# Kernel optimization log

Measured on AMD Instinct MI355X. Metric: run time of the kernel, lower is better.

The kernel has to match this reference:

```python
import jax, jax.numpy as jnp
import numpy as np

MAX_RADIUS = 3.0
NUM_BASIS = 8
NUM_NEIGHBORS = 16.0
N, E, NS, NV, B, D, T, L, HR = 2048, 32768, 32, 16, 8, 32, 32, 2, 64
NW = NS * 2 * NV + NV * 2 * (NS + NV) + NV * 2 * NV  # 3072 per-edge TP weights


def smooth_cutoff(x):
    u = 2.0 * (x - 1.0)
    y = 0.5 * (1.0 - jnp.cos(jnp.pi * u))
    y = jnp.where(u > 0, 0.0, y)
    y = jnp.where(u < -1, 1.0, y)
    return y


def bessel_basis(length):
    # soft_one_hot_linspace(basis='bessel', cutoff=False) * sqrt(NUM_BASIS)
    k = jnp.arange(1, NUM_BASIS + 1, dtype=length.dtype) * jnp.pi
    l = jnp.maximum(length, 1e-9)[..., None]
    return jnp.sqrt(2.0 / MAX_RADIUS) * jnp.sin(k * l / MAX_RADIUS) / l * np.sqrt(NUM_BASIS)


def get_edge_info(x, edge_src, edge_dst):
    n = x.shape[0]
    xr = x.reshape(n, 2, 3)                         # 2 vectors per node
    vec = xr[edge_src] - xr[edge_dst]               # [E,2,3]
    length = jnp.sqrt(jnp.sum(vec * vec, axis=-1) + 1e-12)   # [E,2]
    sh = np.sqrt(3.0) * vec / length[..., None]     # component-normalized l=1 SH
    feat = bessel_basis(length)                     # [E,2,B]
    attr = smooth_cutoff(length / MAX_RADIUS)[..., None] * sh  # [E,2,3]
    return feat.reshape(vec.shape[0], -1), attr


def setup_inputs() -> dict:
    key = jax.random.key(0)
    ks = jax.random.split(key, 20)
    inp = {
        'x': jax.random.normal(ks[0], (N, 6), jnp.float32),
        'batch': jnp.zeros((N,), jnp.int64 if jax.config.jax_enable_x64 else jnp.int32),
        'node_attr': jax.random.randint(ks[1], (N,), 0, T),
        'edge_src': jax.random.randint(ks[2], (E,), 0, N),
        'edge_dst': jax.random.randint(ks[3], (E,), 0, N),
        'emb': jax.random.normal(ks[4], (T, D), jnp.float32),
        'W_uplift': jax.random.normal(ks[5], (NV, 2), jnp.float32),
        'W_sc_s': jax.random.normal(ks[6], (L, NS, D, NS + NV), jnp.float32),
        'W_sc_v': jax.random.normal(ks[7], (L, NV, D, NV), jnp.float32),
        'W_l1_s': jax.random.normal(ks[8], (L, NS, NS), jnp.float32),
        'W_l1_v': jax.random.normal(ks[9], (L, NV, NV), jnp.float32),
        'W_r1': jax.random.normal(ks[10], (L, 2 * B, HR), jnp.float32),
        'W_r2': jax.random.normal(ks[11], (L, HR, NW), jnp.float32),
        'W_l2_s': jax.random.normal(ks[12], (L, NS + NV, NS + NV), jnp.float32),
        'W_l2_v': jax.random.normal(ks[13], (L, NV, NV), jnp.float32),
        'W_si_s': jax.random.normal(ks[14], (L, NS, NS), jnp.float32),
        'W_si_v': jax.random.normal(ks[15], (L, NV, NV), jnp.float32),
        'h': jnp.ones((L,), jnp.float32) * 0.01,
        'mix': jnp.ones((L,), jnp.float32) * 0.5,
    }
    return inp


def reference(x, batch, node_attr, edge_src, edge_dst, emb, W_uplift, W_sc_s, W_sc_v,
              W_l1_s, W_l1_v, W_r1, W_r2, W_l2_s, W_l2_v, W_si_s, W_si_v, h, mix):
    n = x.shape[0]
    a = emb[node_attr]                              # node attr embedding [N,D]
    Q, _ = jnp.linalg.qr(W_uplift)                  # semi-unitary uplift [NV,2]
    y_v = jnp.einsum('ci,nik->nck', Q, x.reshape(n, 2, 3))   # uplift vectors
    y_s = jnp.zeros((n, NS), x.dtype)
    y, y_old = (y_s, y_v), (y_s, y_v)
    n1 = NS * 2 * NV
    n2 = NV * 2 * (NS + NV)
    for i in range(L):
        ef, ea = get_edge_info(x, edge_src, edge_dst)       # [E,2B], [E,2,3]
        ys, yv = y
        # self-connection tensor product (features x node_attr)
        sc_s = jnp.einsum('ni,na,iaj->nj', ys, a, W_sc_s[i]) / np.sqrt(NS * D)
        sc_v = jnp.einsum('nck,na,caj->njk', yv, a, W_sc_v[i]) / np.sqrt(NV * D)
        # lin1
        s1 = ys @ W_l1_s[i] / np.sqrt(NS)
        v1 = jnp.einsum('nck,cj->njk', yv, W_l1_v[i]) / np.sqrt(NV)
        # radial MLP -> per-edge TP weights
        hr = jax.nn.silu(ef @ W_r1[i] / np.sqrt(2 * B))
        w = hr @ W_r2[i] / np.sqrt(HR)                       # [E,NW]
        w_sv = w[:, :n1].reshape(E, NS, 2, NV)
        w_vs = w[:, n1:n1 + n2].reshape(E, NV, 2, NS + NV)
        w_vv = w[:, n1 + n2:].reshape(E, NV, 2, NV)
        s_src, v_src = s1[edge_src], v1[edge_src]
        # edge tensor product: 0e x 1o -> 1o, 1o x 1o -> 0e (dot), 1o x 1o -> 1o (cross)
        e_v = jnp.einsum('esmj,es,emk->ejk', w_sv, s_src, ea) / np.sqrt(NS * 2)
        dots = jnp.einsum('eck,emk->ecm', v_src, ea)
        e_s = jnp.einsum('ecmj,ecm->ej', w_vs, dots) / np.sqrt(NV * 2 * 3)
        crs = jnp.cross(v_src[:, :, None, :], ea[:, None, :, :])  # [E,NV,2,3]
        e_v = e_v + jnp.einsum('ecmj,ecmk->ejk', w_vv, crs) / np.sqrt(NV * 2 * 2)
        # scatter-aggregate over destination nodes
        ns_ = jax.ops.segment_sum(e_s, edge_dst, num_segments=n) / np.sqrt(NUM_NEIGHBORS)
        nv_ = jax.ops.segment_sum(e_v, edge_dst, num_segments=n) / np.sqrt(NUM_NEIGHBORS)
        s2 = ns_ @ W_l2_s[i] / np.sqrt(NS + NV)
        v2 = jnp.einsum('nck,cj->njk', nv_, W_l2_v[i]) / np.sqrt(NV)
        conv_s, conv_v = sc_s + s2, sc_v + v2
        # gate
        g_s = jax.nn.silu(conv_s[:, :NS])
        g_v = jax.nn.sigmoid(conv_s[:, NS:])[:, :, None] * conv_v
        # self-interaction
        si_s = ys @ W_si_s[i] / np.sqrt(NS)
        si_v = jnp.einsum('nck,cj->njk', yv, W_si_v[i]) / np.sqrt(NV)
        # gated leapfrog update
        h2, m = h[i] ** 2, mix[i]
        new_s = 2 * ys - y_old[0] + h2 * (m * g_s + (m - 1) * si_s)
        new_v = 2 * yv - y_old[1] + h2 * (m * g_v + (m - 1) * si_v)
        y_old, y = y, (new_s, new_v)
        x = jnp.einsum('ci,nck->nik', Q, y[1]).reshape(n, 6)  # project back
    return x
```

## Files before the change

kernel.cpp:

```cpp
#include <hip/hip_runtime.h>
#include <hip/hip_bf16.h>
#include <math.h>

#define NN   2048
#define EE   32768
#define NS   32
#define NV   16
#define NB   8
#define DD   32
#define TT   32
#define LL   2
#define HRD  64
#define NWW  3072
#define TPE  128
#define PI_F 3.14159265358979323846f

#define SC_SCS (1.0f/32.0f)
#define SC_SCV 0.04419417382415922f
#define SC_L1S 0.17677669529663687f
#define SC_L1V 0.25f
#define SC_R1  0.25f
#define SC_R2  0.125f
#define SC_ES  0.10206207261596575f
#define SC_EV  0.125f
#define SC_AGG 0.25f
#define SC_L2S 0.14433756729740643f
#define SC_L2V 0.25f
#define SC_SIS 0.17677669529663687f
#define SC_SIV 0.25f

typedef __attribute__((ext_vector_type(8))) short  short8;
typedef __attribute__((ext_vector_type(4))) float  floatx4;

__device__ __forceinline__ floatx4 mfma16(short8 a, short8 b, floatx4 c) {
    return __builtin_amdgcn_mfma_f32_16x16x32_bf16(a, b, c, 0, 0, 0);
}

__device__ __forceinline__ void seg_reduce_store(
        const float (*red)[49], const int* dst_s,
        const int* __restrict__ row_ptr, int ebase,
        int tid, int wave, int lane,
        int* segstart_s, int* wtot_s, int* nseg_s,
        float* __restrict__ outg) {
    int seg_flag = 0, seg_lidx = 0;
    if (tid < TPE) {
        seg_flag = (tid == 0) || (dst_s[tid] != dst_s[tid - 1]);
        unsigned long long m = __ballot(seg_flag != 0);
        if (lane == 0) wtot_s[wave] = (int)__popcll(m);
        seg_lidx = (int)__popcll(m & ((1ull << lane) - 1ull));
    }
    __syncthreads();
    if (seg_flag) segstart_s[seg_lidx + (wave ? wtot_s[0] : 0)] = tid;
    if (tid == 0) {
        int ns = wtot_s[0] + wtot_s[1];
        nseg_s[0] = ns;
        segstart_s[ns] = TPE;
    }
    __syncthreads();
    int nseg = nseg_s[0];
    for (int w = tid; w < nseg * 48; w += 256) {
        int seg = w / 48, c = w - seg * 48;
        int p0 = segstart_s[seg], p1 = segstart_s[seg + 1];
        int d = dst_s[p0];
        float run = 0.f;
        for (int pos = p0; pos < p1; ++pos) run += red[pos][c];
        if (row_ptr[d] >= ebase && row_ptr[d + 1] <= ebase + TPE)
            outg[d * 48 + c] = run;
        else
            atomicAdd(&outg[d * 48 + c], run);
    }
}

__global__ void k_setup(const float* __restrict__ Wup, float* __restrict__ Q,
                        const float* __restrict__ emb,
                        const float* __restrict__ Wscs, const float* __restrict__ Wscv,
                        float* __restrict__ WtS, float* __restrict__ WtV,
                        const float* __restrict__ Wr2, __hip_bfloat16* __restrict__ wr2t,
                        int* __restrict__ deg, int* __restrict__ cursor) {
    int b = blockIdx.x;
    if (b == 0) {
        if (threadIdx.x != 0) return;
        double A[16][2], tau[2];
        for (int i = 0; i < 16; ++i)
            for (int j = 0; j < 2; ++j) A[i][j] = (double)Wup[i*2 + j];
        for (int j = 0; j < 2; ++j) {
            double alpha = A[j][j];
            double xn2 = 0.0;
            for (int i = j + 1; i < 16; ++i) xn2 += A[i][j]*A[i][j];
            if (xn2 == 0.0) {
                tau[j] = 0.0;
            } else {
                double nrm  = sqrt(alpha*alpha + xn2);
                double beta = (alpha >= 0.0) ? -nrm : nrm;
                tau[j] = (beta - alpha) / beta;
                double s = 1.0 / (alpha - beta);
                for (int i = j + 1; i < 16; ++i) A[i][j] *= s;
                A[j][j] = beta;
            }
            for (int k = j + 1; k < 2; ++k) {
                double w = A[j][k];
                for (int i = j + 1; i < 16; ++i) w += A[i][j]*A[i][k];
                w *= tau[j];
                A[j][k] -= w;
                for (int i = j + 1; i < 16; ++i) A[i][k] -= A[i][j]*w;
            }
        }
        double Qm[16][2];
        for (int i = 0; i < 16; ++i)
            for (int j = 0; j < 2; ++j) Qm[i][j] = (i == j) ? 1.0 : 0.0;
        for (int j = 1; j >= 0; --j) {
            for (int k = 0; k < 2; ++k) {
                double w = Qm[j][k];
                for (int i = j + 1; i < 16; ++i) w += A[i][j]*Qm[i][k];
                w *= tau[j];
                Qm[j][k] -= w;
                for (int i = j + 1; i < 16; ++i) Qm[i][k] -= A[i][j]*w;
            }
        }
        for (int i = 0; i < 16; ++i)
            for (int j = 0; j < 2; ++j) Q[i*2 + j] = (float)Qm[i][j];
    } else if (b <= 64) {
        int lt = b - 1;
        int l = lt >> 5, t = lt & 31;
        __shared__ float es[32];
        if (threadIdx.x < 32) es[threadIdx.x] = emb[t*DD + threadIdx.x];
        __syncthreads();
        const float* Ws = Wscs + (size_t)l*NS*DD*48;
        float* oS = WtS + (size_t)(l*TT + t)*NS*48;
        for (int idx = threadIdx.x; idx < NS*48; idx += 256) {
            int i = idx / 48, j = idx % 48;
            float acc = 0.f;
            for (int a = 0; a < 32; ++a) acc += es[a]*Ws[(i*DD + a)*48 + j];
            oS[idx] = acc;
        }
        const float* Wv = Wscv + (size_t)l*NV*DD*NV;
        float* oV = WtV + (size_t)(l*TT + t)*NV*NV;
        for (int idx = threadIdx.x; idx < NV*NV; idx += 256) {
            int c = idx / 16, j = idx % 16;
            float acc = 0.f;
            for (int a = 0; a < 32; ++a) acc += es[a]*Wv[(c*DD + a)*NV + j];
            oV[idx] = acc;
        }
    } else if (b <= 1600) {
        int idx = (b - 65)*256 + threadIdx.x;
        int l = idx / (HRD*NWW);
        int r = idx - l*(HRD*NWW);
        int k = r / NWW;
        int c = r - k*NWW;
        int ch = c >> 6, cc = c & 63, q = cc >> 4, tcc = cc & 15;
        int h = k >> 5, qd = (k >> 3) & 3, j = k & 7;
        size_t dst = (size_t)l*(NWW*HRD)
                   + (size_t)((ch*32 + q*8 + h*4 + qd)*128 + tcc*8 + j);
        wr2t[dst] = __float2bfloat16(Wr2[idx]);
    } else {
        int i = (b - 1601)*256 + threadIdx.x;
        if (i < NN) { deg[i] = 0; cursor[i] = 0; }
    }
}

__global__ void k_hist(const int* __restrict__ edst, int* __restrict__ deg) {
    int e = blockIdx.x*256 + threadIdx.x;
    atomicAdd(&deg[edst[e]], 1);
}

__global__ void k_scan(const int* __restrict__ deg, int* __restrict__ row_ptr) {
    __shared__ int part[256];
    __shared__ int psc[256];
    int t = threadIdx.x;
    int loc[8]; int s = 0;
    for (int k = 0; k < 8; ++k) { loc[k] = deg[t*8 + k]; s += loc[k]; }
    part[t] = s;
    __syncthreads();
    if (t == 0) { int run = 0; for (int i = 0; i < 256; ++i) { psc[i] = run; run += part[i]; } }
    __syncthreads();
    int off = psc[t];
    for (int k = 0; k < 8; ++k) { row_ptr[t*8 + k] = off; off += loc[k]; }
    if (t == 255) row_ptr[2048] = off;
}

__global__ void k_fill(const int* __restrict__ esrc, const int* __restrict__ edst,
                       const int* __restrict__ row_ptr, int* __restrict__ cursor,
                       int* __restrict__ invperm, int* __restrict__ srcs, int* __restrict__ dsts,
                       const float* __restrict__ xin, const float* __restrict__ Q,
                       float* __restrict__ ys0, float* __restrict__ yv0,
                       float* __restrict__ ys1, float* __restrict__ yv1,
                       float* __restrict__ xcur) {
    if (blockIdx.x < 128) {
        int e = blockIdx.x*256 + threadIdx.x;
        int d = edst[e];
        int pos = atomicAdd(&cursor[d], 1);
        int p = row_ptr[d] + pos;
        invperm[e] = p;
        srcs[p] = esrc[e];
        dsts[p] = d;
    } else {
        int n = (blockIdx.x - 128)*256 + threadIdx.x;
        float xl[6];
        for (int i = 0; i < 6; ++i) { xl[i] = xin[n*6 + i]; xcur[n*6 + i] = xl[i]; }
        for (int j = 0; j < 32; ++j) { ys0[n*32 + j] = 0.f; ys1[n*32 + j] = 0.f; }
        for (int c = 0; c < 16; ++c)
            for (int k = 0; k < 3; ++k) {
                float v = Q[c*2 + 0]*xl[k] + Q[c*2 + 1]*xl[3 + k];
                yv0[n*48 + c*3 + k] = v;
                yv1[n*48 + c*3 + k] = v;
            }
    }
}

__global__ void __launch_bounds__(256) k_pre(
        const float* __restrict__ xcur,
        const int* __restrict__ esrc, const int* __restrict__ edst,
        const int* __restrict__ invperm,
        const float* __restrict__ Wr1l,
        __hip_bfloat16* __restrict__ hrg, float* __restrict__ eag,
        const float* __restrict__ ys, const float* __restrict__ yv,
        const float* __restrict__ Wl1s, const float* __restrict__ Wl1v,
        float* __restrict__ s1, float* __restrict__ v1,
        float* __restrict__ nsb, float* __restrict__ nsb2,
        float* __restrict__ nvba, float* __restrict__ nvbb) {
    if (blockIdx.x < 128) {
        __shared__ float Wr1[16*64];
        for (int i = threadIdx.x; i < 16*64; i += 256) Wr1[i] = Wr1l[i];
        __syncthreads();
        int e = blockIdx.x*256 + threadIdx.x;
        int s = esrc[e], d = edst[e];
        int p = invperm[e];
        float ef[16];
        float ea6[6];
        for (int m = 0; m < 2; ++m) {
            float v0 = xcur[s*6 + m*3 + 0] - xcur[d*6 + m*3 + 0];
            float v1_ = xcur[s*6 + m*3 + 1] - xcur[d*6 + m*3 + 1];
            float v2 = xcur[s*6 + m*3 + 2] - xcur[d*6 + m*3 + 2];
            float len = sqrtf(v0*v0 + v1_*v1_ + v2*v2 + 1e-12f);
            float inv = 1.0f/len;
            float theta = len*(PI_F/3.0f);
            float s1v = sinf(theta), c1v = cosf(theta);
            float sc  = 2.3094010767585034f*inv;
            float sp = 0.f, scur = s1v, twoc = 2.f*c1v;
            for (int bq = 0; bq < 8; ++bq) {
                ef[m*8 + bq] = sc*scur;
                float sn = twoc*scur - sp;
                sp = scur; scur = sn;
            }
            float u = 2.0f*(len*(1.0f/3.0f) - 1.0f);
            float cut;
            if (u > 0.f) cut = 0.f;
            else if (u < -1.f) cut = 1.f;
            else cut = 0.5f*(1.0f - cosf(PI_F*u));
            float shs = 1.7320508075688772f*inv*cut;
            ea6[m*3 + 0] = shs*v0;
            ea6[m*3 + 1] = shs*v1_;
            ea6[m*3 + 2] = shs*v2;
        }
        *(float2*)&eag[p*6 + 0] = make_float2(ea6[0], ea6[1]);
        *(float2*)&eag[p*6 + 2] = make_float2(ea6[2], ea6[3]);
        *(float2*)&eag[p*6 + 4] = make_float2(ea6[4], ea6[5]);
        float z[64];
        #pragma unroll
        for (int hh = 0; hh < 64; ++hh) z[hh] = 0.f;
        for (int f = 0; f < 16; ++f) {
            float efv = ef[f];
            #pragma unroll
            for (int hh = 0; hh < 64; ++hh) z[hh] += efv*Wr1[f*64 + hh];
        }
        short8* outp = (short8*)&hrg[(size_t)p*64];
        #pragma unroll
        for (int h8 = 0; h8 < 8; ++h8) {
            __hip_bfloat16 tmp[8];
            #pragma unroll
            for (int j = 0; j < 8; ++j) {
                float zz = z[h8*8 + j]*SC_R1;
                tmp[j] = __float2bfloat16(zz/(1.0f + expf(-zz)));
            }
            outp[h8] = *(short8*)tmp;
        }
    } else {
        int idx = (blockIdx.x - 128)*256 + threadIdx.x;
        int n = idx / 48, r = idx % 48;
        nsb[idx] = 0.f;
        nsb2[idx] = 0.f;
        nvba[idx] = 0.f;
        nvbb[idx] = 0.f;
        if (r < 32) {
            float acc = 0.f;
            for (int i = 0; i < 32; ++i) acc += ys[n*32 + i]*Wl1s[i*32 + r];
            s1[n*32 + r] = acc*SC_L1S;
        }
        int j = r/3, k = r - 3*j;
        float acc = 0.f;
        for (int c = 0; c < 16; ++c) acc += yv[n*48 + c*3 + k]*Wl1v[c*16 + j];
        v1[idx] = acc*SC_L1V;
    }
}

__global__ void __launch_bounds__(256, 3) k_tp(
        const __hip_bfloat16* __restrict__ hrg, const float* __restrict__ eag,
        const float* __restrict__ s1g, const float* __restrict__ v1g,
        const int* __restrict__ srcs, const int* __restrict__ dsts,
        const int* __restrict__ row_ptr,
        const __hip_bfloat16* __restrict__ wr2tl,
        float* __restrict__ nsb, float* __restrict__ nsb2,
        float* __restrict__ nvba, float* __restrict__ nvbb) {
    __shared__ __align__(16) char smem[42240];
    __shared__ float ea_s[TPE][9];
    __shared__ int   src_s[TPE];
    __shared__ int   dst_s[TPE];
    __shared__ int   segstart_s[TPE + 1];
    __shared__ int   wtot_s[2];
    __shared__ int   nseg_s[1];

    int bid = blockIdx.x;
    int region = bid % 3;
    int tile   = bid / 3;
    int ebase  = tile*TPE;
    int tid = threadIdx.x;
    int wave = tid >> 6, lane = tid & 63;
    int tc = tid & 15;
    int quad = lane >> 4;

    if (tid < TPE) { src_s[tid] = srcs[ebase + tid]; dst_s[tid] = dsts[ebase + tid]; }
    for (int i = tid; i < TPE*6; i += 256) ea_s[i/6][i%6] = eag[(size_t)ebase*6 + i];
    __syncthreads();

    const short* hr16 = (const short*)hrg;
    short8 a_lo[2], a_hi[2];
    #pragma unroll
    for (int rt = 0; rt < 2; ++rt) {
        int arow = ebase + (wave*2 + rt)*16 + tc;
        a_lo[rt] = *(const short8*)(hr16 + (size_t)arow*64 + quad*8);
        a_hi[rt] = *(const short8*)(hr16 + (size_t)arow*64 + 32 + quad*8);
    }

    const char* wb = (const char*)wr2tl;
    const float sES = SC_R2*SC_ES*SC_AGG;
    const float sEV = SC_R2*SC_EV*SC_AGG;

    if (region == 0) {
        float (*s1t)[132] = (float(*)[132])smem;
        for (int i = tid; i < TPE*32; i += 256) {
            int e = i >> 5, s = i & 31;
            s1t[s][e] = s1g[src_s[e]*32 + s];
        }
        __syncthreads();

        float accF[2][4][2] = {};
        for (int ci = 0; ci < 16; ++ci) {
            const char* Bc = wb + (size_t)ci*8192 + lane*16;
            #pragma unroll
            for (int q = 0; q < 4; ++q) {
                short8 b_lo = *(const short8*)(Bc + q*2048);
                short8 b_hi = *(const short8*)(Bc + q*2048 + 1024);
                floatx4 c0 = {0.f,0.f,0.f,0.f}, c1 = {0.f,0.f,0.f,0.f};
                c0 = mfma16(a_lo[0], b_lo, c0); c0 = mfma16(a_hi[0], b_hi, c0);
                c1 = mfma16(a_lo[1], b_lo, c1); c1 = mfma16(a_hi[1], b_hi, c1);
                int m = q & 1;
                int sidx = ci*2 + (q >> 1);
                #pragma unroll
                for (int rt = 0; rt < 2; ++rt) {
                    int e0r = (wave*2 + rt)*16 + quad*4;
                    float4 sv = *(const float4*)&s1t[sidx][e0r];
                    floatx4 cc = rt ? c1 : c0;
                    #pragma unroll
                    for (int i = 0; i < 4; ++i)
                        accF[rt][i][m] += cc[i]*((&sv.x)[i]);
                }
            }
        }
        __syncthreads();
        float (*red)[49] = (float(*)[49])smem;
        #pragma unroll
        for (int rt = 0; rt < 2; ++rt) {
            int e0r = (wave*2 + rt)*16 + quad*4;
            #pragma unroll
            for (int i = 0; i < 4; ++i) {
                int pos = e0r + i;
                float f0 = accF[rt][i][0]*sEV, f1 = accF[rt][i][1]*sEV;
                #pragma unroll
                for (int k = 0; k < 3; ++k)
                    red[pos][tc*3 + k] = f0*ea_s[pos][k] + f1*ea_s[pos][3 + k];
            }
        }
        __syncthreads();
        seg_reduce_store((const float(*)[49])smem, dst_s, row_ptr, ebase,
                         tid, wave, lane, segstart_s, wtot_s, nseg_s, nvba);
    } else if (region == 1) {
        float (*dots_t)[132] = (float(*)[132])smem;
        float (*v1t)[132]    = (float(*)[132])(smem + 16896);
        for (int i = tid; i < TPE*48; i += 256) {
            int e = i/48, j = i%48;
            v1t[j][e] = v1g[src_s[e]*48 + j];
        }
        __syncthreads();
        for (int i = tid; i < TPE*32; i += 256) {
            int cm = i >> 7, e = i & (TPE - 1), c = cm >> 1, m = cm & 1;
            dots_t[cm][e] = v1t[c*3+0][e]*ea_s[e][m*3+0]
                          + v1t[c*3+1][e]*ea_s[e][m*3+1]
                          + v1t[c*3+2][e]*ea_s[e][m*3+2];
        }
        __syncthreads();

        float accES[2][4][3] = {};
        for (int ci = 16; ci < 32; ++ci) {
            const char* Bc = wb + (size_t)ci*8192 + lane*16;
            #pragma unroll
            for (int q = 0; q < 4; ++q) {
                short8 b_lo = *(const short8*)(Bc + q*2048);
                short8 b_hi = *(const short8*)(Bc + q*2048 + 1024);
                floatx4 c0 = {0.f,0.f,0.f,0.f}, c1 = {0.f,0.f,0.f,0.f};
                c0 = mfma16(a_lo[0], b_lo, c0); c0 = mfma16(a_hi[0], b_hi, c0);
                c1 = mfma16(a_lo[1], b_lo, c1); c1 = mfma16(a_hi[1], b_hi, c1);
                int u = ci*4 + q - 64;
                int c = (u*10923) >> 16;
                int v6 = u - 6*c;
                int m = (v6 >= 3) ? 1 : 0;
                int g = v6 - 3*m;
                #pragma unroll
                for (int rt = 0; rt < 2; ++rt) {
                    int e0r = (wave*2 + rt)*16 + quad*4;
                    float4 dv = *(const float4*)&dots_t[c*2 + m][e0r];
                    floatx4 cc = rt ? c1 : c0;
                    #pragma unroll
                    for (int i = 0; i < 4; ++i)
                        accES[rt][i][g] += cc[i]*((&dv.x)[i]);
                }
            }
        }
        __syncthreads();
        float (*red)[49] = (float(*)[49])smem;
        #pragma unroll
        for (int rt = 0; rt < 2; ++rt) {
            int e0r = (wave*2 + rt)*16 + quad*4;
            #pragma unroll
            for (int i = 0; i < 4; ++i) {
                int pos = e0r + i;
                red[pos][tc]      = accES[rt][i][0]*sES;
                red[pos][16 + tc] = accES[rt][i][1]*sES;
                red[pos][32 + tc] = accES[rt][i][2]*sES;
            }
        }
        __syncthreads();
        seg_reduce_store((const float(*)[49])smem, dst_s, row_ptr, ebase,
                         tid, wave, lane, segstart_s, wtot_s, nseg_s, nsb);
    } else {
        float (*v1t)[132]  = (float(*)[132])smem;
        float (*dots2)[132] = (float(*)[132])(smem + 25344);
        for (int i = tid; i < TPE*48; i += 256) {
            int e = i/48, j = i%48;
            v1t[j][e] = v1g[src_s[e]*48 + j];
        }
        __syncthreads();
        for (int i = tid; i < 12*TPE; i += 256) {
            int r = i >> 7, e = i & (TPE - 1);
            int c = 10 + (r >> 1), m = r & 1;
            dots2[r][e] = v1t[c*3+0][e]*ea_s[e][m*3+0]
                        + v1t[c*3+1][e]*ea_s[e][m*3+1]
                        + v1t[c*3+2][e]*ea_s[e][m*3+2];
        }
        __syncthreads();

        float accES[2][4][3] = {};
        float accV[2][4][2][3] = {};
        for (int ci = 32; ci < 48; ++ci) {
            const char* Bc = wb + (size_t)ci*8192 + lane*16;
            #pragma unroll
            for (int q = 0; q < 4; ++q) {
                short8 b_lo = *(const short8*)(Bc + q*2048);
                short8 b_hi = *(const short8*)(Bc + q*2048 + 1024);
                floatx4 c0 = {0.f,0.f,0.f,0.f}, c1 = {0.f,0.f,0.f,0.f};
                c0 = mfma16(a_lo[0], b_lo, c0); c0 = mfma16(a_hi[0], b_hi, c0);
                c1 = mfma16(a_lo[1], b_lo, c1); c1 = mfma16(a_hi[1], b_hi, c1);
                if (ci < 40) {
                    int u = ci*4 + q - 64;
                    int c = (u*10923) >> 16;
                    int v6 = u - 6*c;
                    int m = (v6 >= 3) ? 1 : 0;
                    int g = v6 - 3*m;
                    int dr = (c - 10)*2 + m;
                    #pragma unroll
                    for (int rt = 0; rt < 2; ++rt) {
                        int e0r = (wave*2 + rt)*16 + quad*4;
                        float4 dv = *(const float4*)&dots2[dr][e0r];
                        floatx4 cc = rt ? c1 : c0;
                        #pragma unroll
                        for (int i = 0; i < 4; ++i)
                            accES[rt][i][g] += cc[i]*((&dv.x)[i]);
                    }
                } else {
                    int c = ci*2 - 80 + (q >> 1);
                    int m = q & 1;
                    #pragma unroll
                    for (int rt = 0; rt < 2; ++rt) {
                        int e0r = (wave*2 + rt)*16 + quad*4;
                        float4 vx = *(const float4*)&v1t[c*3 + 0][e0r];
                        float4 vy = *(const float4*)&v1t[c*3 + 1][e0r];
                        float4 vz = *(const float4*)&v1t[c*3 + 2][e0r];
                        floatx4 cc = rt ? c1 : c0;
                        #pragma unroll
                        for (int i = 0; i < 4; ++i) {
                            float ww = cc[i];
                            accV[rt][i][m][0] += ww*((&vx.x)[i]);
                            accV[rt][i][m][1] += ww*((&vy.x)[i]);
                            accV[rt][i][m][2] += ww*((&vz.x)[i]);
                        }
                    }
                }
            }
        }
        __syncthreads();
        float (*red)[49] = (float(*)[49])smem;
        #pragma unroll
        for (int rt = 0; rt < 2; ++rt) {
            int e0r = (wave*2 + rt)*16 + quad*4;
            #pragma unroll
            for (int i = 0; i < 4; ++i) {
                int pos = e0r + i;
                red[pos][tc]      = accES[rt][i][0]*sES;
                red[pos][16 + tc] = accES[rt][i][1]*sES;
                red[pos][32 + tc] = accES[rt][i][2]*sES;
            }
        }
        __syncthreads();
        seg_reduce_store((const float(*)[49])smem, dst_s, row_ptr, ebase,
                         tid, wave, lane, segstart_s, wtot_s, nseg_s, nsb2);
        __syncthreads();
        #pragma unroll
        for (int rt = 0; rt < 2; ++rt) {
            int e0r = (wave*2 + rt)*16 + quad*4;
            #pragma unroll
            for (int i = 0; i < 4; ++i) {
                int pos = e0r + i;
                float u00 = accV[rt][i][0][0], u01 = accV[rt][i][0][1], u02 = accV[rt][i][0][2];
                float u10 = accV[rt][i][1][0], u11 = accV[rt][i][1][1], u12 = accV[rt][i][1][2];
                float a0 = ea_s[pos][0], a1 = ea_s[pos][1], a2 = ea_s[pos][2];
                float b0 = ea_s[pos][3], b1 = ea_s[pos][4], b2 = ea_s[pos][5];
                red[pos][tc*3 + 0] = (u01*a2 - u02*a1 + u11*b2 - u12*b1)*sEV;
                red[pos][tc*3 + 1] = (u02*a0 - u00*a2 + u12*b0 - u10*b2)*sEV;
                red[pos][tc*3 + 2] = (u00*a1 - u01*a0 + u10*b1 - u11*b0)*sEV;
            }
        }
        __syncthreads();
        seg_reduce_store((const float(*)[49])smem, dst_s, row_ptr, ebase,
                         tid, wave, lane, segstart_s, wtot_s, nseg_s, nvbb);
    }
}

__global__ void __launch_bounds__(256) k_nodepost(
        const float* __restrict__ ysC, const float* __restrict__ yvC,
        float* __restrict__ ysO, float* __restrict__ yvO,
        const float* __restrict__ nsb, const float* __restrict__ nsb2,
        const float* __restrict__ nvba, const float* __restrict__ nvbb,
        const int* __restrict__ nattr,
        const float* __restrict__ WtSl, const float* __restrict__ WtVl,
        const float* __restrict__ Wl2s, const float* __restrict__ Wl2v,
        const float* __restrict__ Wsis, const float* __restrict__ Wsiv,
        const float* __restrict__ harr, const float* __restrict__ mixarr, int l,
        float* __restrict__ xcur, float* __restrict__ xout2,
        const float* __restrict__ Qg) {
    int wave = threadIdx.x >> 6, lane = threadIdx.x & 63;
    int n = blockIdx.x*4 + wave;
    __shared__ float ys_s[4][32], yv_s[4][48], ns_s[4][48], nv_s[4][48];
    __shared__ float cs_s[4][48], nvo_s[4][48];

    if (lane < 32) ys_s[wave][lane] = ysC[n*32 + lane];
    if (lane < 48) {
        yv_s[wave][lane] = yvC[n*48 + lane];
        ns_s[wave][lane] = nsb[n*48 + lane] + nsb2[n*48 + lane];
        nv_s[wave][lane] = nvba[n*48 + lane] + nvbb[n*48 + lane];
    }
    __syncthreads();
    int t = nattr[n];
    const float* WtSn = WtSl + (size_t)t*NS*48;
    const float* WtVn = WtVl + (size_t)t*NV*NV;
    float hv = harr[l];
    float h2 = hv*hv, mx = mixarr[l];

    if (lane < 48) {
        float sc = 0.f, s2 = 0.f;
        for (int i = 0; i < 32; ++i) sc += ys_s[wave][i]*WtSn[i*48 + lane];
        for (int c = 0; c < 48; ++c) s2 += ns_s[wave][c]*Wl2s[c*48 + lane];
        cs_s[wave][lane] = sc*SC_SCS + s2*SC_L2S;
    }
    __syncthreads();
    if (lane < 48) {
        int j = lane/3, k = lane - 3*j;
        float scv = 0.f, v2 = 0.f, siv = 0.f;
        for (int c = 0; c < 16; ++c) {
            float yvv = yv_s[wave][c*3 + k];
            scv += yvv*WtVn[c*16 + j];
            v2  += nv_s[wave][c*3 + k]*Wl2v[c*16 + j];
            siv += yvv*Wsiv[c*16 + j];
        }
        float convv = scv*SC_SCV + v2*SC_L2V;
        siv *= SC_SIV;
        float gate = 1.f/(1.f + expf(-cs_s[wave][32 + j]));
        float gv = gate*convv;
        float nvnew = 2.f*yv_s[wave][lane] - yvO[n*48 + lane] + h2*(mx*gv + (mx - 1.f)*siv);
        nvo_s[wave][lane] = nvnew;
        yvO[n*48 + lane] = nvnew;
    }
    if (lane < 32) {
        float sis = 0.f;
        for (int i = 0; i < 32; ++i) sis += ys_s[wave][i]*Wsis[i*32 + lane];
        sis *= SC_SIS;
        float cs = cs_s[wave][lane];
        float gs = cs/(1.f + expf(-cs));
        float nsnew = 2.f*ys_s[wave][lane] - ysO[n*32 + lane] + h2*(mx*gs + (mx - 1.f)*sis);
        ysO[n*32 + lane] = nsnew;
    }
    __syncthreads();
    if (lane < 6) {
        int i = lane/3, k = lane - 3*(lane/3);
        float acc = 0.f;
        for (int c = 0; c < 16; ++c) acc += Qg[c*2 + i]*nvo_s[wave][c*3 + k];
        xcur[n*6 + lane]  = acc;
        xout2[n*6 + lane] = acc;
    }
}

extern "C" void kernel_launch(void* const* d_in, const int* in_sizes, int n_in,
                              void* d_out, int out_size, void* d_ws, size_t ws_size,
                              hipStream_t stream) {
    const float* x_in  = (const float*)d_in[0];
    const int*   nattr = (const int*)  d_in[2];
    const int*   esrc  = (const int*)  d_in[3];
    const int*   edst  = (const int*)  d_in[4];
    const float* emb   = (const float*)d_in[5];
    const float* Wup   = (const float*)d_in[6];
    const float* Wscs  = (const float*)d_in[7];
    const float* Wscv  = (const float*)d_in[8];
    const float* Wl1s  = (const float*)d_in[9];
    const float* Wl1v  = (const float*)d_in[10];
    const float* Wr1   = (const float*)d_in[11];
    const float* Wr2   = (const float*)d_in[12];
    const float* Wl2s  = (const float*)d_in[13];
    const float* Wl2v  = (const float*)d_in[14];
    const float* Wsis  = (const float*)d_in[15];
    const float* Wsiv  = (const float*)d_in[16];
    const float* harr  = (const float*)d_in[17];
    const float* mixar = (const float*)d_in[18];
    float* out = (float*)d_out;

    float* ws = (float*)d_ws;
    size_t off = 0;
    float* Q    = ws + off; off += 32;
    float* WtS  = ws + off; off += (size_t)LL*TT*NS*48;
    float* WtV  = ws + off; off += (size_t)LL*TT*NV*NV;
    float* ys0  = ws + off; off += (size_t)NN*32;
    float* yv0  = ws + off; off += (size_t)NN*48;
    float* ys1  = ws + off; off += (size_t)NN*32;
    float* yv1  = ws + off; off += (size_t)NN*48;
    float* xcur = ws + off; off += (size_t)NN*6;
    float* s1   = ws + off; off += (size_t)NN*32;
    float* v1   = ws + off; off += (size_t)NN*48;
    float* nsb  = ws + off; off += (size_t)NN*48;
    float* nsb2 = ws + off; off += (size_t)NN*48;
    float* nvba = ws + off; off += (size_t)NN*48;
    float* nvbb = ws + off; off += (size_t)NN*48;
    float* eab  = ws + off; off += (size_t)EE*6;
    off = (off + 3) & ~(size_t)3;
    __hip_bfloat16* hrb  = (__hip_bfloat16*)(ws + off); off += (size_t)EE*64/2;
    __hip_bfloat16* wr2t = (__hip_bfloat16*)(ws + off); off += (size_t)LL*NWW*HRD/2;
    int* deg     = (int*)(ws + off); off += NN;
    int* cursor  = (int*)(ws + off); off += NN;
    int* row_ptr = (int*)(ws + off); off += NN + 1;
    int* invperm = (int*)(ws + off); off += EE;
    int* srcs    = (int*)(ws + off); off += EE;
    int* dsts    = (int*)(ws + off); off += EE;

    k_setup<<<1609, 256, 0, stream>>>(Wup, Q, emb, Wscs, Wscv, WtS, WtV, Wr2, wr2t,
                                      deg, cursor);
    k_hist<<<EE/256, 256, 0, stream>>>(edst, deg);
    k_scan<<<1, 256, 0, stream>>>(deg, row_ptr);
    k_fill<<<136, 256, 0, stream>>>(esrc, edst, row_ptr, cursor, invperm, srcs, dsts,
                                    x_in, Q, ys0, yv0, ys1, yv1, xcur);

    float* curS = ys0; float* curV = yv0;
    float* oldS = ys1; float* oldV = yv1;
    for (int l = 0; l < LL; ++l) {
        k_pre<<<512, 256, 0, stream>>>(xcur, esrc, edst, invperm,
                                       Wr1 + (size_t)l*16*64, hrb, eab,
                                       curS, curV, Wl1s + (size_t)l*32*32,
                                       Wl1v + (size_t)l*16*16, s1, v1,
                                       nsb, nsb2, nvba, nvbb);
        k_tp<<<3*EE/TPE, 256, 0, stream>>>(hrb, eab, s1, v1, srcs, dsts, row_ptr,
                                           wr2t + (size_t)l*NWW*HRD,
                                           nsb, nsb2, nvba, nvbb);
        float* xo2 = (l == LL - 1) ? out : xcur;
        k_nodepost<<<NN/4, 256, 0, stream>>>(curS, curV, oldS, oldV,
                                             nsb, nsb2, nvba, nvbb, nattr,
                                             WtS + (size_t)l*TT*NS*48, WtV + (size_t)l*TT*NV*NV,
                                             Wl2s + (size_t)l*48*48, Wl2v + (size_t)l*16*16,
                                             Wsis + (size_t)l*32*32, Wsiv + (size_t)l*16*16,
                                             harr, mixar, l, xcur, xo2, Q);
        float* ts = curS; curS = oldS; oldS = ts;
        float* tv = curV; curV = oldV; oldV = tv;
    }
}
```

Measured before the change: 260.0 us.

## Fuse edge preprocessing into tensor-product kernel and node linear into nodepost

```diff
diff --git a/kernel.cpp b/kernel.cpp
--- a/kernel.cpp
+++ b/kernel.cpp
@@ -180,17 +180,20 @@
 
 __global__ void k_fill(const int* __restrict__ esrc, const int* __restrict__ edst,
                        const int* __restrict__ row_ptr, int* __restrict__ cursor,
-                       int* __restrict__ invperm, int* __restrict__ srcs, int* __restrict__ dsts,
+                       int* __restrict__ srcs, int* __restrict__ dsts,
                        const float* __restrict__ xin, const float* __restrict__ Q,
                        float* __restrict__ ys0, float* __restrict__ yv0,
                        float* __restrict__ ys1, float* __restrict__ yv1,
-                       float* __restrict__ xcur) {
+                       float* __restrict__ xcur,
+                       const float* __restrict__ Wl1v0,
+                       float* __restrict__ s1, float* __restrict__ v1,
+                       float* __restrict__ nsb, float* __restrict__ nsb2,
+                       float* __restrict__ nvba, float* __restrict__ nvbb) {
     if (blockIdx.x < 128) {
         int e = blockIdx.x*256 + threadIdx.x;
         int d = edst[e];
         int pos = atomicAdd(&cursor[d], 1);
         int p = row_ptr[d] + pos;
-        invperm[e] = p;
         srcs[p] = esrc[e];
         dsts[p] = d;
     } else {
@@ -198,35 +201,61 @@
         float xl[6];
         for (int i = 0; i < 6; ++i) { xl[i] = xin[n*6 + i]; xcur[n*6 + i] = xl[i]; }
         for (int j = 0; j < 32; ++j) { ys0[n*32 + j] = 0.f; ys1[n*32 + j] = 0.f; }
+        float yvv[48];
         for (int c = 0; c < 16; ++c)
             for (int k = 0; k < 3; ++k) {
                 float v = Q[c*2 + 0]*xl[k] + Q[c*2 + 1]*xl[3 + k];
+                yvv[c*3 + k] = v;
                 yv0[n*48 + c*3 + k] = v;
                 yv1[n*48 + c*3 + k] = v;
             }
-    }
-}
-
-__global__ void __launch_bounds__(256) k_pre(
+        for (int r = 0; r < 32; ++r) s1[n*32 + r] = 0.f;
+        for (int r = 0; r < 48; ++r) {
+            int j = r/3, k = r - 3*j;
+            float a = 0.f;
+            for (int c = 0; c < 16; ++c) a += yvv[c*3 + k]*Wl1v0[c*16 + j];
+            v1[n*48 + r] = a*SC_L1V;
+            nsb[n*48 + r] = 0.f; nsb2[n*48 + r] = 0.f;
+            nvba[n*48 + r] = 0.f; nvbb[n*48 + r] = 0.f;
+        }
+    }
+}
+
+__global__ void __launch_bounds__(256, 3) k_tp(
         const float* __restrict__ xcur,
-        const int* __restrict__ esrc, const int* __restrict__ edst,
-        const int* __restrict__ invperm,
+        const int* __restrict__ srcs, const int* __restrict__ dsts,
+        const int* __restrict__ row_ptr,
         const float* __restrict__ Wr1l,
-        __hip_bfloat16* __restrict__ hrg, float* __restrict__ eag,
-        const float* __restrict__ ys, const float* __restrict__ yv,
-        const float* __restrict__ Wl1s, const float* __restrict__ Wl1v,
-        float* __restrict__ s1, float* __restrict__ v1,
+        const __hip_bfloat16* __restrict__ wr2tl,
+        const float* __restrict__ s1g, const float* __restrict__ v1g,
         float* __restrict__ nsb, float* __restrict__ nsb2,
         float* __restrict__ nvba, float* __restrict__ nvbb) {
-    if (blockIdx.x < 128) {
-        __shared__ float Wr1[16*64];
-        for (int i = threadIdx.x; i < 16*64; i += 256) Wr1[i] = Wr1l[i];
-        __syncthreads();
-        int e = blockIdx.x*256 + threadIdx.x;
-        int s = esrc[e], d = edst[e];
-        int p = invperm[e];
-        float ef[16];
-        float ea6[6];
+    __shared__ __align__(16) char smem[42240];
+    __shared__ float ea_s[TPE][9];
+    __shared__ int   src_s[TPE];
+    __shared__ int   dst_s[TPE];
+    __shared__ int   segstart_s[TPE + 1];
+    __shared__ int   wtot_s[2];
+    __shared__ int   nseg_s[1];
+
+    int bid = blockIdx.x;
+    int region = bid % 3;
+    int tile   = bid / 3;
+    int ebase  = tile*TPE;
+    int tid = threadIdx.x;
+    int wave = tid >> 6, lane = tid & 63;
+    int tc = tid & 15;
+    int quad = lane >> 4;
+
+    float* ef_lds  = (float*)smem;
+    float* Wr1_lds = (float*)(smem + 8448);
+    __hip_bfloat16* hr_lds = (__hip_bfloat16*)(smem + 12544);
+
+    if (tid < TPE) { src_s[tid] = srcs[ebase + tid]; dst_s[tid] = dsts[ebase + tid]; }
+    for (int i = tid; i < 16*64; i += 256) Wr1_lds[i] = Wr1l[i];
+
+    if (tid < TPE) {
+        int s = src_s[tid], d = dst_s[tid];
         for (int m = 0; m < 2; ++m) {
             float v0 = xcur[s*6 + m*3 + 0] - xcur[d*6 + m*3 + 0];
             float v1_ = xcur[s*6 + m*3 + 1] - xcur[d*6 + m*3 + 1];
@@ -238,7 +267,7 @@
             float sc  = 2.3094010767585034f*inv;
             float sp = 0.f, scur = s1v, twoc = 2.f*c1v;
             for (int bq = 0; bq < 8; ++bq) {
-                ef[m*8 + bq] = sc*scur;
+                ef_lds[(m*8 + bq)*132 + tid] = sc*scur;
                 float sn = twoc*scur - sp;
                 sp = scur; scur = sn;
             }
@@ -248,88 +277,45 @@
             else if (u < -1.f) cut = 1.f;
             else cut = 0.5f*(1.0f - cosf(PI_F*u));
             float shs = 1.7320508075688772f*inv*cut;
-            ea6[m*3 + 0] = shs*v0;
-            ea6[m*3 + 1] = shs*v1_;
-            ea6[m*3 + 2] = shs*v2;
-        }
-        *(float2*)&eag[p*6 + 0] = make_float2(ea6[0], ea6[1]);
-        *(float2*)&eag[p*6 + 2] = make_float2(ea6[2], ea6[3]);
-        *(float2*)&eag[p*6 + 4] = make_float2(ea6[4], ea6[5]);
-        float z[64];
+            ea_s[tid][m*3 + 0] = shs*v0;
+            ea_s[tid][m*3 + 1] = shs*v1_;
+            ea_s[tid][m*3 + 2] = shs*v2;
+        }
+    }
+    __syncthreads();
+
+    {
+        int e = tid >> 1, h = tid & 1;
+        float z[32];
         #pragma unroll
-        for (int hh = 0; hh < 64; ++hh) z[hh] = 0.f;
+        for (int k = 0; k < 32; ++k) z[k] = 0.f;
         for (int f = 0; f < 16; ++f) {
-            float efv = ef[f];
-            #pragma unroll
-            for (int hh = 0; hh < 64; ++hh) z[hh] += efv*Wr1[f*64 + hh];
-        }
-        short8* outp = (short8*)&hrg[(size_t)p*64];
+            float efv = ef_lds[f*132 + e];
+            #pragma unroll
+            for (int k = 0; k < 32; ++k) z[k] += efv*Wr1_lds[f*64 + h*32 + k];
+        }
         #pragma unroll
-        for (int h8 = 0; h8 < 8; ++h8) {
+        for (int q8 = 0; q8 < 4; ++q8) {
             __hip_bfloat16 tmp[8];
             #pragma unroll
             for (int j = 0; j < 8; ++j) {
-                float zz = z[h8*8 + j]*SC_R1;
+                float zz = z[q8*8 + j]*SC_R1;
                 tmp[j] = __float2bfloat16(zz/(1.0f + expf(-zz)));
             }
-            outp[h8] = *(short8*)tmp;
-        }
-    } else {
-        int idx = (blockIdx.x - 128)*256 + threadIdx.x;
-        int n = idx / 48, r = idx % 48;
-        nsb[idx] = 0.f;
-        nsb2[idx] = 0.f;
-        nvba[idx] = 0.f;
-        nvbb[idx] = 0.f;
-        if (r < 32) {
-            float acc = 0.f;
-            for (int i = 0; i < 32; ++i) acc += ys[n*32 + i]*Wl1s[i*32 + r];
-            s1[n*32 + r] = acc*SC_L1S;
-        }
-        int j = r/3, k = r - 3*j;
-        float acc = 0.f;
-        for (int c = 0; c < 16; ++c) acc += yv[n*48 + c*3 + k]*Wl1v[c*16 + j];
-        v1[idx] = acc*SC_L1V;
-    }
-}
-
-__global__ void __launch_bounds__(256, 3) k_tp(
-        const __hip_bfloat16* __restrict__ hrg, const float* __restrict__ eag,
-        const float* __restrict__ s1g, const float* __restrict__ v1g,
-        const int* __restrict__ srcs, const int* __restrict__ dsts,
-        const int* __restrict__ row_ptr,
-        const __hip_bfloat16* __restrict__ wr2tl,
-        float* __restrict__ nsb, float* __restrict__ nsb2,
-        float* __restrict__ nvba, float* __restrict__ nvbb) {
-    __shared__ __align__(16) char smem[42240];
-    __shared__ float ea_s[TPE][9];
-    __shared__ int   src_s[TPE];
-    __shared__ int   dst_s[TPE];
-    __shared__ int   segstart_s[TPE + 1];
-    __shared__ int   wtot_s[2];
-    __shared__ int   nseg_s[1];
-
-    int bid = blockIdx.x;
-    int region = bid % 3;
-    int tile   = bid / 3;
-    int ebase  = tile*TPE;
-    int tid = threadIdx.x;
-    int wave = tid >> 6, lane = tid & 63;
-    int tc = tid & 15;
-    int quad = lane >> 4;
-
-    if (tid < TPE) { src_s[tid] = srcs[ebase + tid]; dst_s[tid] = dsts[ebase + tid]; }
-    for (int i = tid; i < TPE*6; i += 256) ea_s[i/6][i%6] = eag[(size_t)ebase*6 + i];
-    __syncthreads();
-
-    const short* hr16 = (const short*)hrg;
+            *(short8*)&hr_lds[e*72 + h*32 + q8*8] = *(short8*)tmp;
+        }
+    }
+    __syncthreads();
+
+    const short* hrp = (const short*)(smem + 12544);
     short8 a_lo[2], a_hi[2];
     #pragma unroll
     for (int rt = 0; rt < 2; ++rt) {
-        int arow = ebase + (wave*2 + rt)*16 + tc;
-        a_lo[rt] = *(const short8*)(hr16 + (size_t)arow*64 + quad*8);
-        a_hi[rt] = *(const short8*)(hr16 + (size_t)arow*64 + 32 + quad*8);
-    }
+        int row = (wave*2 + rt)*16 + tc;
+        a_lo[rt] = *(const short8*)(hrp + row*72 + quad*8);
+        a_hi[rt] = *(const short8*)(hrp + row*72 + 32 + quad*8);
+    }
+    __syncthreads();
 
     const char* wb = (const char*)wr2tl;
     const float sES = SC_R2*SC_ES*SC_AGG;
@@ -555,11 +541,16 @@
         const float* __restrict__ Wsis, const float* __restrict__ Wsiv,
         const float* __restrict__ harr, const float* __restrict__ mixarr, int l,
         float* __restrict__ xcur, float* __restrict__ xout2,
-        const float* __restrict__ Qg) {
+        const float* __restrict__ Qg,
+        const float* __restrict__ Wl1sN, const float* __restrict__ Wl1vN,
+        float* __restrict__ s1, float* __restrict__ v1,
+        float* __restrict__ znsb, float* __restrict__ znsb2,
+        float* __restrict__ znvba, float* __restrict__ znvbb,
+        int do_next) {
     int wave = threadIdx.x >> 6, lane = threadIdx.x & 63;
     int n = blockIdx.x*4 + wave;
     __shared__ float ys_s[4][32], yv_s[4][48], ns_s[4][48], nv_s[4][48];
-    __shared__ float cs_s[4][48], nvo_s[4][48];
+    __shared__ float cs_s[4][48], nvo_s[4][48], nsn_s[4][32];
 
     if (lane < 32) ys_s[wave][lane] = ysC[n*32 + lane];
     if (lane < 48) {
@@ -605,6 +596,7 @@
         float cs = cs_s[wave][lane];
         float gs = cs/(1.f + expf(-cs));
         float nsnew = 2.f*ys_s[wave][lane] - ysO[n*32 + lane] + h2*(mx*gs + (mx - 1.f)*sis);
+        nsn_s[wave][lane] = nsnew;
         ysO[n*32 + lane] = nsnew;
     }
     __syncthreads();
@@ -614,6 +606,21 @@
         for (int c = 0; c < 16; ++c) acc += Qg[c*2 + i]*nvo_s[wave][c*3 + k];
         xcur[n*6 + lane]  = acc;
         xout2[n*6 + lane] = acc;
+    }
+    if (do_next) {
+        if (lane < 32) {
+            float a = 0.f;
+            for (int i = 0; i < 32; ++i) a += nsn_s[wave][i]*Wl1sN[i*32 + lane];
+            s1[n*32 + lane] = a*SC_L1S;
+        }
+        if (lane < 48) {
+            int j = lane/3, k = lane - 3*j;
+            float a = 0.f;
+            for (int c = 0; c < 16; ++c) a += nvo_s[wave][c*3 + k]*Wl1vN[c*16 + j];
+            v1[n*48 + lane] = a*SC_L1V;
+            znsb[n*48 + lane] = 0.f; znsb2[n*48 + lane] = 0.f;
+            znvba[n*48 + lane] = 0.f; znvbb[n*48 + lane] = 0.f;
+        }
     }
 }
 
@@ -656,14 +663,11 @@
     float* nsb2 = ws + off; off += (size_t)NN*48;
     float* nvba = ws + off; off += (size_t)NN*48;
     float* nvbb = ws + off; off += (size_t)NN*48;
-    float* eab  = ws + off; off += (size_t)EE*6;
     off = (off + 3) & ~(size_t)3;
-    __hip_bfloat16* hrb  = (__hip_bfloat16*)(ws + off); off += (size_t)EE*64/2;
     __hip_bfloat16* wr2t = (__hip_bfloat16*)(ws + off); off += (size_t)LL*NWW*HRD/2;
     int* deg     = (int*)(ws + off); off += NN;
     int* cursor  = (int*)(ws + off); off += NN;
     int* row_ptr = (int*)(ws + off); off += NN + 1;
-    int* invperm = (int*)(ws + off); off += EE;
     int* srcs    = (int*)(ws + off); off += EE;
     int* dsts    = (int*)(ws + off); off += EE;
 
@@ -671,27 +675,28 @@
                                       deg, cursor);
     k_hist<<<EE/256, 256, 0, stream>>>(edst, deg);
     k_scan<<<1, 256, 0, stream>>>(deg, row_ptr);
-    k_fill<<<136, 256, 0, stream>>>(esrc, edst, row_ptr, cursor, invperm, srcs, dsts,
-                                    x_in, Q, ys0, yv0, ys1, yv1, xcur);
+    k_fill<<<136, 256, 0, stream>>>(esrc, edst, row_ptr, cursor, srcs, dsts,
+                                    x_in, Q, ys0, yv0, ys1, yv1, xcur,
+                                    Wl1v, s1, v1, nsb, nsb2, nvba, nvbb);
 
     float* curS = ys0; float* curV = yv0;
     float* oldS = ys1; float* oldV = yv1;
     for (int l = 0; l < LL; ++l) {
-        k_pre<<<512, 256, 0, stream>>>(xcur, esrc, edst, invperm,
-                                       Wr1 + (size_t)l*16*64, hrb, eab,
-                                       curS, curV, Wl1s + (size_t)l*32*32,
-                                       Wl1v + (size_t)l*16*16, s1, v1,
-                                       nsb, nsb2, nvba, nvbb);
-        k_tp<<<3*EE/TPE, 256, 0, stream>>>(hrb, eab, s1, v1, srcs, dsts, row_ptr,
+        k_tp<<<3*EE/TPE, 256, 0, stream>>>(xcur, srcs, dsts, row_ptr,
+                                           Wr1 + (size_t)l*16*64,
                                            wr2t + (size_t)l*NWW*HRD,
-                                           nsb, nsb2, nvba, nvbb);
+                                           s1, v1, nsb, nsb2, nvba, nvbb);
         float* xo2 = (l == LL - 1) ? out : xcur;
+        int lN = (l + 1 < LL) ? (l + 1) : l;
         k_nodepost<<<NN/4, 256, 0, stream>>>(curS, curV, oldS, oldV,
                                              nsb, nsb2, nvba, nvbb, nattr,
                                              WtS + (size_t)l*TT*NS*48, WtV + (size_t)l*TT*NV*NV,
                                              Wl2s + (size_t)l*48*48, Wl2v + (size_t)l*16*16,
                                              Wsis + (size_t)l*32*32, Wsiv + (size_t)l*16*16,
-                                             harr, mixar, l, xcur, xo2, Q);
+                                             harr, mixar, l, xcur, xo2, Q,
+                                             Wl1s + (size_t)lN*32*32, Wl1v + (size_t)lN*16*16,
+                                             s1, v1, nsb, nsb2, nvba, nvbb,
+                                             (l + 1 < LL) ? 1 : 0);
         float* ts = curS; curS = oldS; oldS = ts;
         float* tv = curV; curV = oldV; oldV = tv;
     }
```

Measured after the change: 280.2 us. 7.8% more time.
